# Optimization experiments

Measured on AMD Instinct MI355X. Metric: run time of the kernel, lower is better.

The kernel has to match this reference:

```python
import jax, jax.numpy as jnp
import numpy as np
from jax import lax

V, E, H = 128, 32, 128  # vocab, embed_dim, hidden_size
B, S = 4, 512


def setup_inputs() -> dict:
    key = jax.random.key(0)
    ks = jax.random.split(key, 14)
    sc = 0.05
    return {
        "x": jax.random.randint(ks[0], (B, S), 0, V),
        "emb": jax.random.normal(ks[1], (V, E), jnp.float32) * sc,
        "W_ih": jax.random.normal(ks[2], (4 * H, E), jnp.float32) * sc,
        "W_hh": jax.random.normal(ks[3], (4 * H, H), jnp.float32) * sc,
        "b_ih": jax.random.normal(ks[4], (4 * H,), jnp.float32) * sc,
        "b_hh": jax.random.normal(ks[5], (4 * H,), jnp.float32) * sc,
        "Wq": jax.random.normal(ks[6], (H, H), jnp.float32) * sc,
        "bq": jax.random.normal(ks[7], (H,), jnp.float32) * sc,
        "Wk": jax.random.normal(ks[8], (H, H), jnp.float32) * sc,
        "bk": jax.random.normal(ks[9], (H,), jnp.float32) * sc,
        "v": jax.random.normal(ks[10], (H,), jnp.float32) * sc,
        "Wf": jax.random.normal(ks[11], (V, 2 * H), jnp.float32) * sc,
        "bf": jax.random.normal(ks[12], (V,), jnp.float32) * sc,
    }


def _lstm(e, W_ih, W_hh, b_ih, b_hh):
    # e: (B, S, E) -> outputs (B, S, H); PyTorch gate order i, f, g, o
    b, s, _ = e.shape
    h0 = jnp.zeros((b, H), e.dtype)
    c0 = jnp.zeros((b, H), e.dtype)
    bias = b_ih + b_hh

    def step(carry, xt):
        h, c = carry
        g = xt @ W_ih.T + h @ W_hh.T + bias  # (B, 4H)
        i, f, gg, o = jnp.split(g, 4, axis=-1)
        c = jax.nn.sigmoid(f) * c + jax.nn.sigmoid(i) * jnp.tanh(gg)
        h = jax.nn.sigmoid(o) * jnp.tanh(c)
        return (h, c), h

    (hT, cT), hs = lax.scan(step, (h0, c0), jnp.swapaxes(e, 0, 1))
    return jnp.swapaxes(hs, 0, 1), hT, cT


def reference(x, emb, W_ih, W_hh, b_ih, b_hh, Wq, bq, Wk, bk, v, Wf, bf):
    e = emb[x]  # (B, S, E)
    out, hT, cT = _lstm(e, W_ih, W_hh, b_ih, b_hh)  # (B, S, H)
    s = out.shape[1]
    q = out @ Wq.T + bq  # (B, S, H)
    k = out @ Wk.T + bk  # (B, S, H)
    # Bahdanau additive scores: v^T tanh(q_t + k_i) -> (B, S, S)
    t = jnp.tanh(q[:, :, None, :] + k[:, None, :, :])  # (B, S, S, H)
    scores = jnp.einsum('bsth,h->bst', t, v)
    mask = jnp.tril(jnp.ones((s, s), bool))
    scores = jnp.where(mask[None], scores, -jnp.inf)
    w = jax.nn.softmax(scores, axis=-1)
    ctx = jnp.einsum('bst,bth->bsh', w, out)
    logits = jnp.concatenate([out, ctx], axis=-1) @ Wf.T + bf  # (B, S, V)
    return logits, hT, cT
```

## Files before the change

### kernel.cpp

```cpp
#include <hip/hip_runtime.h>

#define Vn 128
#define En 32
#define Hn 128
#define Bn 4
#define Sn 512
#define G4H 512

typedef _Float16 half8 __attribute__((ext_vector_type(8)));
typedef float    floatx4 __attribute__((ext_vector_type(4)));

__device__ __forceinline__ float fsigmoid(float x) {
    return 1.0f / (1.0f + __expf(-x));
}

__device__ __forceinline__ float ftanh(float x) {
    float ax = fabsf(x);
    float e  = __expf(2.0f * ax);
    float t  = 1.0f - 2.0f / (e + 1.0f);
    return copysignf(t, x);
}

__global__ __launch_bounds__(512) void k_gtab(
        const float* __restrict__ emb, const float* __restrict__ Wih,
        const float* __restrict__ bih, const float* __restrict__ bhh,
        float* __restrict__ Gtab) {
    int v = blockIdx.x;
    int g = threadIdx.x;
    __shared__ float e[En];
    if (g < En) e[g] = emb[v * En + g];
    __syncthreads();
    const float4* wr = (const float4*)(Wih + g * En);
    float acc = bih[g] + bhh[g];
#pragma unroll
    for (int i = 0; i < En / 4; i++) {
        float4 w4 = wr[i];
        acc += w4.x * e[4*i] + w4.y * e[4*i+1] + w4.z * e[4*i+2] + w4.w * e[4*i+3];
    }
    Gtab[v * G4H + (g & 127) * 4 + (g >> 7)] = acc;
}

__global__ __attribute__((amdgpu_flat_work_group_size(512, 512),
                          amdgpu_waves_per_eu(2, 2)))
void k_lstm(
        const float* __restrict__ Whh, const float* __restrict__ Gtab,
        const int* __restrict__ x,
        float* __restrict__ out, float* __restrict__ hT, float* __restrict__ cT) {
    int tid = threadIdx.x;
    int wv  = tid >> 6;
    int l   = tid & 63;
    int cn  = l & 15;
    int kg  = l >> 4;
    int cb  = l & 3;
    int jr  = l >> 2;
    int bb  = l & 3;
    int aj  = 16 * wv + jr;

    bool r1 = (l >> 2) & 1;
    bool r2 = (l >> 2) & 2;

    __shared__ int xb[4][520];
    __shared__ alignas(16) _Float16 hbuf[2][4][144];

    for (int i = tid; i < Bn * Sn; i += 512) xb[i >> 9][i & 511] = x[i];
    for (int i = tid; i < 2 * 4 * 144; i += 512) ((_Float16*)hbuf)[i] = (_Float16)0.0f;

    half8 af[4][4];
#pragma unroll
    for (int g = 0; g < 4; g++) {
#pragma unroll
        for (int kc = 0; kc < 4; kc++) {
            int row = g * Hn + 16 * wv + cn;
            int kb  = kc * 32 + kg * 8;
            const float4* p = (const float4*)(Whh + row * Hn + kb);
            float4 lo = p[0], hi = p[1];
            half8 a = { (_Float16)lo.x, (_Float16)lo.y, (_Float16)lo.z, (_Float16)lo.w,
                        (_Float16)hi.x, (_Float16)hi.y, (_Float16)hi.z, (_Float16)hi.w };
            af[g][kc] = a;
        }
    }

    float c_ = 0.f, h_ = 0.f;
    __syncthreads();

    float4 gx4 = *(const float4*)(Gtab + xb[bb][0] * G4H + aj * 4);

    int cur = 0;
    for (int s = 0; s < Sn; s++) {
        half8 bf[4];
#pragma unroll
        for (int kc = 0; kc < 4; kc++)
            bf[kc] = *(const half8*)&hbuf[cur][cb][kc * 32 + kg * 8];

        floatx4 d[4];
#pragma unroll
        for (int g = 0; g < 4; g++) {
            floatx4 acc = { 0.f, 0.f, 0.f, 0.f };
#pragma unroll
            for (int kc = 0; kc < 4; kc++)
                acc = __builtin_amdgcn_mfma_f32_16x16x32_f16(af[g][kc], bf[kc], acc, 0, 0, 0);
            d[g] = acc;
        }

        int sn = (s + 1 < Sn) ? s + 1 : s;
        float4 ngx = *(const float4*)(Gtab + xb[bb][sn] * G4H + aj * 4);

        float ex[4];
#pragma unroll
        for (int g = 0; g < 4; g++) {
            float lo = r1 ? d[g][1] : d[g][0];
            float hi = r1 ? d[g][3] : d[g][2];
            ex[g] = r2 ? hi : lo;
        }

        float gi = gx4.x + ex[0];
        float gf = gx4.y + ex[1];
        float gg = gx4.z + ex[2];
        float go = gx4.w + ex[3];
        c_ = fsigmoid(gf) * c_ + fsigmoid(gi) * ftanh(gg);
        h_ = fsigmoid(go) * ftanh(c_);

        out[bb * Sn * Hn + s * Hn + aj] = h_;
        hbuf[cur ^ 1][bb][aj] = (_Float16)h_;

        gx4 = ngx;
        asm volatile("s_waitcnt lgkmcnt(0)\n\ts_barrier" ::: "memory");
        cur ^= 1;
    }
    hT[bb * Hn + aj] = h_;
    cT[bb * Hn + aj] = c_;
}

__global__ __launch_bounds__(256) void k_qk(
        const float* __restrict__ out, const float* __restrict__ Wq,
        const float* __restrict__ bq, const float* __restrict__ Wk,
        const float* __restrict__ bk, float* __restrict__ qo, float* __restrict__ ko) {
    int bs  = blockIdx.x;
    int tid = threadIdx.x;
    __shared__ float o[Hn];
    if (tid < Hn) o[tid] = out[bs * Hn + tid];
    __syncthreads();
    int h = tid & 127;
    const float* Wm = (tid < Hn) ? Wq : Wk;
    const float* bm = (tid < Hn) ? bq : bk;
    const float4* wr = (const float4*)(Wm + h * Hn);
    float acc = bm[h];
#pragma unroll
    for (int i = 0; i < Hn / 4; i++) {
        float4 w4 = wr[i];
        acc += w4.x * o[4*i] + w4.y * o[4*i+1] + w4.z * o[4*i+2] + w4.w * o[4*i+3];
    }
    float* dst = (tid < Hn) ? qo : ko;
    dst[bs * Hn + h] = acc;
}

__global__ __launch_bounds__(512) void k_attn(
        const float* __restrict__ qo, const float* __restrict__ ko,
        const float* __restrict__ vvec, const float* __restrict__ out,
        float* __restrict__ ctx) {
    int b   = blockIdx.x >> 9;
    int t   = blockIdx.x & (Sn - 1);
    int tid = threadIdx.x;
    int wv  = tid >> 6;
    __shared__ float qs[Hn];
    __shared__ float vs[Hn];
    __shared__ float sc[Sn];
    __shared__ float wmax[8];
    __shared__ float wsum[8];
    __shared__ float part[16][Hn];

    if (tid < Hn) {
        qs[tid] = qo[(b * Sn + t) * Hn + tid];
        vs[tid] = vvec[tid];
    }
    __syncthreads();

    float a = -1e30f;
    if (tid <= t) {
        const float4* kr = (const float4*)(ko + (b * Sn + tid) * Hn);
        float s = 0.0f;
#pragma unroll
        for (int u = 0; u < Hn / 4; u++) {
            float4 k4 = kr[u];
            s += vs[4*u]   * ftanh(qs[4*u]   + k4.x);
            s += vs[4*u+1] * ftanh(qs[4*u+1] + k4.y);
            s += vs[4*u+2] * ftanh(qs[4*u+2] + k4.z);
            s += vs[4*u+3] * ftanh(qs[4*u+3] + k4.w);
        }
        sc[tid] = s;
        a = s;
    }
#pragma unroll
    for (int off = 32; off > 0; off >>= 1) a = fmaxf(a, __shfl_xor(a, off));
    if ((tid & 63) == 0) wmax[wv] = a;
    __syncthreads();
    float m = wmax[0];
#pragma unroll
    for (int r = 1; r < 8; r++) m = fmaxf(m, wmax[r]);

    float ev = 0.0f;
    if (tid <= t) {
        ev = __expf(sc[tid] - m);
        sc[tid] = ev;
    }
    float ssum = ev;
#pragma unroll
    for (int off = 32; off > 0; off >>= 1) ssum += __shfl_xor(ssum, off);
    if ((tid & 63) == 0) wsum[wv] = ssum;
    __syncthreads();
    float tot = wsum[0];
#pragma unroll
    for (int r = 1; r < 8; r++) tot += wsum[r];
    float inv = 1.0f / tot;

    int hq = tid & 31;
    int is = tid >> 5;
    float4 acc = {0.0f, 0.0f, 0.0f, 0.0f};
    const float4* ob = (const float4*)(out + b * Sn * Hn);
    for (int i = is; i <= t; i += 16) {
        float s = sc[i];
        float4 o4 = ob[i * (Hn / 4) + hq];
        acc.x += s * o4.x; acc.y += s * o4.y;
        acc.z += s * o4.z; acc.w += s * o4.w;
    }
    ((float4*)part[is])[hq] = acc;
    __syncthreads();
    if (tid < Hn) {
        float sum2 = 0.0f;
#pragma unroll
        for (int r = 0; r < 16; r++) sum2 += part[r][tid];
        ctx[(b * Sn + t) * Hn + tid] = sum2 * inv;
    }
}

__global__ __launch_bounds__(128) void k_final(
        const float* __restrict__ out, const float* __restrict__ ctx,
        const float* __restrict__ Wf, const float* __restrict__ bf,
        float* __restrict__ logits) {
    int bs  = blockIdx.x;
    int tid = threadIdx.x;
    __shared__ float oc[2 * Hn];
    oc[tid]      = out[bs * Hn + tid];
    oc[tid + Hn] = ctx[bs * Hn + tid];
    __syncthreads();
    const float4* wr = (const float4*)(Wf + tid * 2 * Hn);
    float acc = bf[tid];
#pragma unroll
    for (int i = 0; i < (2 * Hn) / 4; i++) {
        float4 w4 = wr[i];
        acc += w4.x * oc[4*i] + w4.y * oc[4*i+1] + w4.z * oc[4*i+2] + w4.w * oc[4*i+3];
    }
    logits[bs * Vn + tid] = acc;
}

extern "C" void kernel_launch(void* const* d_in, const int* in_sizes, int n_in,
                              void* d_out, int out_size, void* d_ws, size_t ws_size,
                              hipStream_t stream) {
    const int*   x   = (const int*)d_in[0];
    const float* emb = (const float*)d_in[1];
    const float* Wih = (const float*)d_in[2];
    const float* Whh = (const float*)d_in[3];
    const float* bih = (const float*)d_in[4];
    const float* bhh = (const float*)d_in[5];
    const float* Wq  = (const float*)d_in[6];
    const float* bq  = (const float*)d_in[7];
    const float* Wk  = (const float*)d_in[8];
    const float* bk  = (const float*)d_in[9];
    const float* v   = (const float*)d_in[10];
    const float* Wf  = (const float*)d_in[11];
    const float* bf  = (const float*)d_in[12];

    float* logits = (float*)d_out;
    float* hT     = logits + Bn * Sn * Vn;
    float* cT     = hT + Bn * Hn;

    float* ws   = (float*)d_ws;
    float* Gtab = ws;
    float* outb = ws + 65536;
    float* qo   = ws + 65536 + 262144;
    float* ko   = ws + 65536 + 2 * 262144;
    float* ctx  = ws + 65536 + 3 * 262144;

    k_gtab<<<Vn, 512, 0, stream>>>(emb, Wih, bih, bhh, Gtab);
    k_lstm<<<1, 512, 0, stream>>>(Whh, Gtab, x, outb, hT, cT);
    k_qk<<<Bn * Sn, 256, 0, stream>>>(outb, Wq, bq, Wk, bk, qo, ko);
    k_attn<<<Bn * Sn, 512, 0, stream>>>(qo, ko, v, outb, ctx);
    k_final<<<Bn * Sn, 128, 0, stream>>>(outb, ctx, Wf, bf, logits);
}
```

Before: 530.2 us.

## Fuse query and output projections into attention kernel, streamline LSTM loop

Folds the per-row query projection and the final output projection into the attention kernel, splitting each dot product across four thread groups with a shared-memory reduction. This removes the k_final launch and the q/ctx round trips through global memory, and k_k now computes only keys. The LSTM loop now pre-scales token indices into byte offsets, pads the index array so the next-step load needs no clamp, uses pointer increments and unroll 2. The tanh helper drops its abs/copysign form, which may overflow to inf for large inputs but still evaluates to the right limit.

```diff
diff --git a/kernel.cpp b/kernel.cpp
--- a/kernel.cpp
+++ b/kernel.cpp
@@ -15,10 +15,8 @@
 }
 
 __device__ __forceinline__ float ftanh(float x) {
-    float ax = fabsf(x);
-    float e  = __expf(2.0f * ax);
-    float t  = 1.0f - 2.0f / (e + 1.0f);
-    return copysignf(t, x);
+    float e = __expf(2.0f * x);
+    return 1.0f - 2.0f / (e + 1.0f);
 }
 
 __global__ __launch_bounds__(512) void k_gtab(
@@ -62,7 +60,8 @@
     __shared__ int xb[4][520];
     __shared__ alignas(16) _Float16 hbuf[2][4][144];
 
-    for (int i = tid; i < Bn * Sn; i += 512) xb[i >> 9][i & 511] = x[i];
+    for (int i = tid; i < Bn * Sn; i += 512) xb[i >> 9][i & 511] = x[i] * 2048;
+    if (tid < 4) xb[tid][512] = 0;
     for (int i = tid; i < 2 * 4 * 144; i += 512) ((_Float16*)hbuf)[i] = (_Float16)0.0f;
 
     half8 af[4][4];
@@ -81,16 +80,18 @@
     }
 
     float c_ = 0.f, h_ = 0.f;
-    __syncthreads();
-
-    float4 gx4 = *(const float4*)(Gtab + xb[bb][0] * G4H + aj * 4);
-
-    int cur = 0;
+    const char* gbase = (const char*)Gtab + aj * 16;
+    float* outp = out + bb * Sn * Hn + aj;
+    __syncthreads();
+
+    float4 gx4 = *(const float4*)(gbase + xb[bb][0]);
+
+#pragma unroll 2
     for (int s = 0; s < Sn; s++) {
         half8 bf[4];
 #pragma unroll
         for (int kc = 0; kc < 4; kc++)
-            bf[kc] = *(const half8*)&hbuf[cur][cb][kc * 32 + kg * 8];
+            bf[kc] = *(const half8*)&hbuf[s & 1][cb][kc * 32 + kg * 8];
 
         floatx4 d[4];
 #pragma unroll
@@ -102,8 +103,7 @@
             d[g] = acc;
         }
 
-        int sn = (s + 1 < Sn) ? s + 1 : s;
-        float4 ngx = *(const float4*)(Gtab + xb[bb][sn] * G4H + aj * 4);
+        float4 ngx = *(const float4*)(gbase + xb[bb][s + 1]);
 
         float ex[4];
 #pragma unroll
@@ -120,59 +120,73 @@
         c_ = fsigmoid(gf) * c_ + fsigmoid(gi) * ftanh(gg);
         h_ = fsigmoid(go) * ftanh(c_);
 
-        out[bb * Sn * Hn + s * Hn + aj] = h_;
-        hbuf[cur ^ 1][bb][aj] = (_Float16)h_;
+        *outp = h_;  outp += Hn;
+        hbuf[(s & 1) ^ 1][bb][aj] = (_Float16)h_;
 
         gx4 = ngx;
         asm volatile("s_waitcnt lgkmcnt(0)\n\ts_barrier" ::: "memory");
-        cur ^= 1;
     }
     hT[bb * Hn + aj] = h_;
     cT[bb * Hn + aj] = c_;
 }
 
-__global__ __launch_bounds__(256) void k_qk(
-        const float* __restrict__ out, const float* __restrict__ Wq,
-        const float* __restrict__ bq, const float* __restrict__ Wk,
-        const float* __restrict__ bk, float* __restrict__ qo, float* __restrict__ ko) {
+__global__ __launch_bounds__(128) void k_k(
+        const float* __restrict__ out, const float* __restrict__ Wk,
+        const float* __restrict__ bk, float* __restrict__ ko) {
     int bs  = blockIdx.x;
     int tid = threadIdx.x;
     __shared__ float o[Hn];
-    if (tid < Hn) o[tid] = out[bs * Hn + tid];
-    __syncthreads();
-    int h = tid & 127;
-    const float* Wm = (tid < Hn) ? Wq : Wk;
-    const float* bm = (tid < Hn) ? bq : bk;
-    const float4* wr = (const float4*)(Wm + h * Hn);
-    float acc = bm[h];
+    o[tid] = out[bs * Hn + tid];
+    __syncthreads();
+    const float4* wr = (const float4*)(Wk + tid * Hn);
+    float acc = bk[tid];
 #pragma unroll
     for (int i = 0; i < Hn / 4; i++) {
         float4 w4 = wr[i];
         acc += w4.x * o[4*i] + w4.y * o[4*i+1] + w4.z * o[4*i+2] + w4.w * o[4*i+3];
     }
-    float* dst = (tid < Hn) ? qo : ko;
-    dst[bs * Hn + h] = acc;
+    ko[bs * Hn + tid] = acc;
 }
 
 __global__ __launch_bounds__(512) void k_attn(
-        const float* __restrict__ qo, const float* __restrict__ ko,
-        const float* __restrict__ vvec, const float* __restrict__ out,
-        float* __restrict__ ctx) {
+        const float* __restrict__ ko, const float* __restrict__ vvec,
+        const float* __restrict__ out,
+        const float* __restrict__ Wq, const float* __restrict__ bq,
+        const float* __restrict__ Wf, const float* __restrict__ bf,
+        float* __restrict__ logits) {
     int b   = blockIdx.x >> 9;
     int t   = blockIdx.x & (Sn - 1);
     int tid = threadIdx.x;
     int wv  = tid >> 6;
     __shared__ float qs[Hn];
     __shared__ float vs[Hn];
+    __shared__ float oc[2 * Hn];
     __shared__ float sc[Sn];
     __shared__ float wmax[8];
     __shared__ float wsum[8];
     __shared__ float part[16][Hn];
 
     if (tid < Hn) {
-        qs[tid] = qo[(b * Sn + t) * Hn + tid];
+        oc[tid] = out[(b * Sn + t) * Hn + tid];
         vs[tid] = vvec[tid];
     }
+    __syncthreads();
+
+    {
+        int h = tid & 127, kq = tid >> 7;
+        const float4* wr = (const float4*)(Wq + h * Hn + kq * 32);
+        const float* ob = oc + kq * 32;
+        float a = 0.0f;
+#pragma unroll
+        for (int i = 0; i < 8; i++) {
+            float4 w4 = wr[i];
+            a += w4.x * ob[4*i] + w4.y * ob[4*i+1] + w4.z * ob[4*i+2] + w4.w * ob[4*i+3];
+        }
+        part[kq][h] = a;
+    }
+    __syncthreads();
+    if (tid < Hn)
+        qs[tid] = bq[tid] + part[0][tid] + part[1][tid] + part[2][tid] + part[3][tid];
     __syncthreads();
 
     float a = -1e30f;
@@ -216,10 +230,10 @@
     int hq = tid & 31;
     int is = tid >> 5;
     float4 acc = {0.0f, 0.0f, 0.0f, 0.0f};
-    const float4* ob = (const float4*)(out + b * Sn * Hn);
+    const float4* ob4 = (const float4*)(out + b * Sn * Hn);
     for (int i = is; i <= t; i += 16) {
         float s = sc[i];
-        float4 o4 = ob[i * (Hn / 4) + hq];
+        float4 o4 = ob4[i * (Hn / 4) + hq];
         acc.x += s * o4.x; acc.y += s * o4.y;
         acc.z += s * o4.z; acc.w += s * o4.w;
     }
@@ -229,28 +243,26 @@
         float sum2 = 0.0f;
 #pragma unroll
         for (int r = 0; r < 16; r++) sum2 += part[r][tid];
-        ctx[(b * Sn + t) * Hn + tid] = sum2 * inv;
-    }
-}
-
-__global__ __launch_bounds__(128) void k_final(
-        const float* __restrict__ out, const float* __restrict__ ctx,
-        const float* __restrict__ Wf, const float* __restrict__ bf,
-        float* __restrict__ logits) {
-    int bs  = blockIdx.x;
-    int tid = threadIdx.x;
-    __shared__ float oc[2 * Hn];
-    oc[tid]      = out[bs * Hn + tid];
-    oc[tid + Hn] = ctx[bs * Hn + tid];
-    __syncthreads();
-    const float4* wr = (const float4*)(Wf + tid * 2 * Hn);
-    float acc = bf[tid];
-#pragma unroll
-    for (int i = 0; i < (2 * Hn) / 4; i++) {
-        float4 w4 = wr[i];
-        acc += w4.x * oc[4*i] + w4.y * oc[4*i+1] + w4.z * oc[4*i+2] + w4.w * oc[4*i+3];
-    }
-    logits[bs * Vn + tid] = acc;
+        oc[Hn + tid] = sum2 * inv;
+    }
+    __syncthreads();
+
+    {
+        int v = tid & 127, kq = tid >> 7;
+        const float4* wr = (const float4*)(Wf + v * 2 * Hn + kq * 64);
+        const float* ob = oc + kq * 64;
+        float a2 = 0.0f;
+#pragma unroll
+        for (int i = 0; i < 16; i++) {
+            float4 w4 = wr[i];
+            a2 += w4.x * ob[4*i] + w4.y * ob[4*i+1] + w4.z * ob[4*i+2] + w4.w * ob[4*i+3];
+        }
+        part[kq][v] = a2;
+    }
+    __syncthreads();
+    if (tid < Hn)
+        logits[(b * Sn + t) * Vn + tid] =
+            bf[tid] + part[0][tid] + part[1][tid] + part[2][tid] + part[3][tid];
 }
 
 extern "C" void kernel_launch(void* const* d_in, const int* in_sizes, int n_in,
@@ -277,13 +289,10 @@
     float* ws   = (float*)d_ws;
     float* Gtab = ws;
     float* outb = ws + 65536;
-    float* qo   = ws + 65536 + 262144;
-    float* ko   = ws + 65536 + 2 * 262144;
-    float* ctx  = ws + 65536 + 3 * 262144;
+    float* ko   = ws + 65536 + 262144;
 
     k_gtab<<<Vn, 512, 0, stream>>>(emb, Wih, bih, bhh, Gtab);
     k_lstm<<<1, 512, 0, stream>>>(Whh, Gtab, x, outb, hT, cT);
-    k_qk<<<Bn * Sn, 256, 0, stream>>>(outb, Wq, bq, Wk, bk, qo, ko);
-    k_attn<<<Bn * Sn, 512, 0, stream>>>(qo, ko, v, outb, ctx);
-    k_final<<<Bn * Sn, 128, 0, stream>>>(outb, ctx, Wf, bf, logits);
-}
+    k_k<<<Bn * Sn, 128, 0, stream>>>(outb, Wk, bk, ko);
+    k_attn<<<Bn * Sn, 512, 0, stream>>>(ko, v, outb, Wq, bq, Wf, bf, logits);
+}
```

Result: faster. 518.0 us (-2.3%).
